# Kernel optimization log

Hardware: AMD Instinct MI355X
Metric: run time of the kernel (lower is better)

The kernel has to match this reference:

```python
import jax, jax.numpy as jnp
import numpy as np
import math

EMBED_DIM = 1024
NUM_HEADS = 16
HEAD_DIM = EMBED_DIM // NUM_HEADS


def setup_inputs() -> dict:
    key = jax.random.key(0)
    ks = jax.random.split(key, 5)
    x = jax.random.normal(ks[0], (4, 2048, EMBED_DIM), dtype=jnp.float32)
    # Linear params (torch nn.Linear: y = x @ W.T + b); init scale ~ 1/sqrt(fan_in)
    s = 1.0 / math.sqrt(EMBED_DIM)
    qkv_w = jax.random.uniform(ks[1], (3 * EMBED_DIM, EMBED_DIM), jnp.float32, -s, s)
    qkv_b = jax.random.uniform(ks[2], (3 * EMBED_DIM,), jnp.float32, -s, s)
    proj_w = jax.random.uniform(ks[3], (EMBED_DIM, EMBED_DIM), jnp.float32, -s, s)
    proj_b = jax.random.uniform(ks[4], (EMBED_DIM,), jnp.float32, -s, s)
    return {"x": x, "qkv_w": qkv_w, "qkv_b": qkv_b, "proj_w": proj_w, "proj_b": proj_b}


def reference(x, qkv_w, qkv_b, proj_w, proj_b):
    bsz, num_tokens, dim = x.shape
    qkv = x @ qkv_w.T + qkv_b  # [B, S, 3*D]
    qkv = qkv.reshape(bsz, num_tokens, 3, NUM_HEADS, HEAD_DIM)
    qkv = jnp.transpose(qkv, (2, 0, 3, 1, 4))  # [3, B, H, S, hd]
    q, k, v = qkv[0], qkv[1], qkv[2]
    scale = 1.0 / math.sqrt(HEAD_DIM)
    attn_scores = jnp.einsum('bhqd,bhkd->bhqk', q, k) * scale  # [B, H, S, S]
    attn = jax.nn.softmax(attn_scores, axis=-1)
    out = jnp.einsum('bhqk,bhkd->bhqd', attn, v)  # [B, H, S, hd]
    out = jnp.transpose(out, (0, 2, 1, 3)).reshape(bsz, num_tokens, dim)
    out = out @ proj_w.T + proj_b
    return out
```

## Files before the change

### kernel.cpp

```cpp
#include <hip/hip_runtime.h>
#include <stdint.h>

#define DEVICE static __device__ __forceinline__

typedef __bf16 bf16x8 __attribute__((ext_vector_type(8)));
typedef float f32x4 __attribute__((ext_vector_type(4)));

#define AS1 __attribute__((address_space(1)))
#define AS3 __attribute__((address_space(3)))

DEVICE void g2l16(const void* gptr, void* lptr) {
  __builtin_amdgcn_global_load_lds((AS1 uint32_t*)(uintptr_t)gptr,
                                   (AS3 uint32_t*)(uint32_t)(uintptr_t)lptr,
                                   16, 0, 0);
}

DEVICE float b2f(ushort h) {
  union { uint32_t u; float f; } v;
  v.u = ((uint32_t)h) << 16;
  return v.f;
}
DEVICE ushort f2b(float f) {
  union { float f; uint32_t u; } v;
  v.f = f;
  uint32_t u = v.u;
  return (ushort)((u + 0x7FFFu + ((u >> 16) & 1u)) >> 16);
}

#if defined(__has_builtin) && __has_builtin(__builtin_amdgcn_exp2f)
DEVICE float fast_exp2(float x) { return __builtin_amdgcn_exp2f(x); }
#else
extern "C" __device__ float __ocml_native_exp2_f32(float);
DEVICE float fast_exp2(float x) { return __ocml_native_exp2_f32(x); }
#endif

#define QSCALE 0.1803368801111244f

DEVICE int kperm(int x) {
  return (x & 0x23) | ((x & 0x18) >> 1) | ((x & 0x4) << 2);
}

__global__ void detect_dtype(const ushort* __restrict__ xu, int* __restrict__ flag) {
  __shared__ int bad;
  if (threadIdx.x == 0) bad = 0;
  __syncthreads();
  int mybad = 0;
#pragma unroll
  for (int j = 0; j < 8; ++j) {
    const int i = threadIdx.x * 8 + j;
    const ushort u = xu[2 * i];
    const int e = (u >> 7) & 0xFF;
    if (!(e == 0 || (e >= 96 && e <= 160))) mybad++;
  }
  atomicAdd(&bad, mybad);
  __syncthreads();
  if (threadIdx.x == 0) *flag = (bad > 512) ? 1 : 0;
}

__global__ void convert_bf16(const void* __restrict__ src, ushort* __restrict__ dst,
                             int n, const int* __restrict__ flag) {
  const bool isf32 = (*flag != 0);
  const int n8 = n >> 3;
  for (int i = blockIdx.x * blockDim.x + threadIdx.x; i < n8;
       i += gridDim.x * blockDim.x) {
    ushort pk[8];
    if (isf32) {
      const float4 a = ((const float4*)src)[2 * i];
      const float4 b = ((const float4*)src)[2 * i + 1];
      pk[0] = f2b(a.x); pk[1] = f2b(a.y); pk[2] = f2b(a.z); pk[3] = f2b(a.w);
      pk[4] = f2b(b.x); pk[5] = f2b(b.y); pk[6] = f2b(b.z); pk[7] = f2b(b.w);
      *(uint4*)&dst[8 * i] = *(const uint4*)pk;
    } else {
      *(uint4*)&dst[8 * i] = ((const uint4*)src)[i];
    }
  }
}

template <int MODE, int GN>
__global__ __launch_bounds__(256)
void gemm_bt(const ushort* __restrict__ A, const ushort* __restrict__ W,
             const ushort* __restrict__ bias, ushort* __restrict__ O0,
             ushort* __restrict__ O1, ushort* __restrict__ O2,
             int M, int N, int K, const int* __restrict__ flag)
{
  __shared__ union SM {
    struct { ushort As[128 * 64]; ushort Bs[128 * 64]; } s;
    ushort Ct[128 * 136];
  } sm;

  const int tid = threadIdx.x;
  const int lane = tid & 63;
  const int wave = tid >> 6;
  const int quad = lane >> 4;
  const int lo = lane & 15;

  const int lin = blockIdx.y * gridDim.x + blockIdx.x;
  const int per = GN * gridDim.y;
  const int grp = lin / per;
  const int w   = lin % per;
  const int bxn = grp * GN + (w % GN);
  const int bym = w / GN;
  const int m0 = bym * 128;
  const int n0 = bxn * 128;

  const int wm = (wave >> 1) * 64;
  const int wn = (wave & 1) * 64;

  f32x4 acc[4][4] = {};

  for (int k0 = 0; k0 < K; k0 += 64) {
    __syncthreads();
#pragma unroll
    for (int i = 0; i < 4; ++i) {
      const int c = tid + 256 * i;
      const int row = c >> 3;
      const int kc = (c & 7) << 3;
      g2l16(A + (size_t)(m0 + row) * K + k0 + kc,
            (char*)sm.s.As + ((wave << 6) + (i << 8)) * 16);
      g2l16(W + (size_t)(n0 + row) * K + k0 + kc,
            (char*)sm.s.Bs + ((wave << 6) + (i << 8)) * 16);
    }
    __syncthreads();

#pragma unroll
    for (int ks = 0; ks < 2; ++ks) {
      bf16x8 af[4], bfr[4];
#pragma unroll
      for (int t = 0; t < 4; ++t) {
        af[t]  = *(const bf16x8*)&sm.s.As[(wm + t * 16 + lo) * 64 + ks * 32 + quad * 8];
        bfr[t] = *(const bf16x8*)&sm.s.Bs[(wn + t * 16 + lo) * 64 + ks * 32 + quad * 8];
      }
#pragma unroll
      for (int mt = 0; mt < 4; ++mt)
#pragma unroll
        for (int nt = 0; nt < 4; ++nt)
          acc[mt][nt] = __builtin_amdgcn_mfma_f32_16x16x32_bf16(
              af[mt], bfr[nt], acc[mt][nt], 0, 0, 0);
    }
  }

  if (MODE == 0) {
    const int which = n0 >> 10;
    if (which == 2) {
#pragma unroll
      for (int nt = 0; nt < 4; ++nt) {
        const int n = n0 + wn + nt * 16 + lo;
        const float bv2 = b2f(bias[n]);
        const int h = (n >> 6) & 15;
        const int d = n & 63;
#pragma unroll
        for (int mt = 0; mt < 4; ++mt) {
          const int mb = m0 + wm + mt * 16 + quad * 4;
          const int b = mb >> 11, s0 = mb & 2047;
          ushort pk[4];
#pragma unroll
          for (int r = 0; r < 4; ++r) pk[r] = f2b(acc[mt][nt][r] + bv2);
          *(uint2*)&O2[((size_t)(b * 16 + h) * 64 + d) * 2048 + s0] =
              *(const uint2*)pk;
        }
      }
    } else {
      const float qs = (which == 0) ? QSCALE : 1.0f;
      ushort* __restrict__ dst = (which == 0) ? O0 : O1;
      __syncthreads();
#pragma unroll
      for (int nt = 0; nt < 4; ++nt) {
        const int n = n0 + wn + nt * 16 + lo;
        const float bv2 = b2f(bias[n]);
#pragma unroll
        for (int mt = 0; mt < 4; ++mt)
#pragma unroll
          for (int r = 0; r < 4; ++r)
            sm.Ct[(wm + mt * 16 + quad * 4 + r) * 136 + wn + nt * 16 + lo] =
                f2b((acc[mt][nt][r] + bv2) * qs);
      }
      __syncthreads();
#pragma unroll
      for (int i = 0; i < 8; ++i) {
        const int c = tid + 256 * i;
        const int nch = c & 15;
        const int ml = c >> 4;
        const int n = n0 + nch * 8;
        const int h = (n >> 6) & 15;
        const int d = n & 63;
        const int mg = m0 + ml;
        const int b = mg >> 11;
        int s = mg & 2047;
        if (which == 1) s = (s & ~63) | kperm(s & 63);
        const uint4 val = *(const uint4*)&sm.Ct[ml * 136 + nch * 8];
        *(uint4*)&dst[(((size_t)(b * 16 + h) * 2048 + s) << 6) + d] = val;
      }
    }
  } else {
    const bool f32out = (*flag != 0);
    float* Of = (float*)O0;
#pragma unroll
    for (int nt = 0; nt < 4; ++nt) {
      const int n = n0 + wn + nt * 16 + lo;
      const float bv2 = b2f(bias[n]);
#pragma unroll
      for (int mt = 0; mt < 4; ++mt)
#pragma unroll
        for (int r = 0; r < 4; ++r) {
          const int m = m0 + wm + mt * 16 + quad * 4 + r;
          const float val = acc[mt][nt][r] + bv2;
          if (f32out) Of[(size_t)m * N + n] = val;
          else        O0[(size_t)m * N + n] = f2b(val);
        }
    }
  }
}

__global__ __launch_bounds__(256, 4)
void attn_fwd(const ushort* __restrict__ qp, const ushort* __restrict__ kp,
              const ushort* __restrict__ vp, ushort* __restrict__ o)
{
  __shared__ ushort Qs[128 * 64];
  __shared__ ushort Ks[64 * 64];
  __shared__ ushort Vt[64 * 64];

  const int tid = threadIdx.x;
  const int lane = tid & 63;
  const int wave = tid >> 6;
  const int quad = lane >> 4;
  const int lo = lane & 15;
  const int bh = blockIdx.y;
  const int q0 = blockIdx.x * 128;

  const ushort* Qg = qp + (size_t)bh * 2048 * 64;
  const ushort* Kg = kp + (size_t)bh * 2048 * 64;
  const ushort* Vg = vp + (size_t)bh * 64 * 2048;

#pragma unroll
  for (int i = 0; i < 4; ++i) {
    const int c = tid + 256 * i;
    const int row = c >> 3;
    const int kc = (c & 7) << 3;
    g2l16(Qg + (size_t)(q0 + row) * 64 + kc,
          (char*)Qs + ((wave << 6) + (i << 8)) * 16);
  }
  __syncthreads();

  bf16x8 qf[2][2];
#pragma unroll
  for (int mt = 0; mt < 2; ++mt)
#pragma unroll
    for (int ks = 0; ks < 2; ++ks)
      qf[mt][ks] = *(const bf16x8*)&Qs[(wave * 32 + mt * 16 + lo) * 64 + ks * 32 + quad * 8];

  bf16x8 ones;
#pragma unroll
  for (int j = 0; j < 8; ++j) ones[j] = (__bf16)1.0f;

  f32x4 oacc[2][4] = {};
  f32x4 sumacc[2] = {};

  for (int j0 = 0; j0 < 2048; j0 += 64) {
    __syncthreads();
#pragma unroll
    for (int i = 0; i < 2; ++i) {
      const int c = tid + 256 * i;
      const int row = c >> 3;
      const int kc = (c & 7) << 3;
      g2l16(Kg + (size_t)(j0 + row) * 64 + kc,
            (char*)Ks + ((wave << 6) + (i << 8)) * 16);
      g2l16(Vg + (size_t)row * 2048 + j0 + kc,
            (char*)Vt + ((wave << 6) + (i << 8)) * 16);
    }
    __syncthreads();

    f32x4 sacc[2][4] = {};
#pragma unroll
    for (int ks = 0; ks < 2; ++ks) {
#pragma unroll
      for (int nt = 0; nt < 4; ++nt) {
        const bf16x8 kf = *(const bf16x8*)&Ks[(nt * 16 + lo) * 64 + ks * 32 + quad * 8];
#pragma unroll
        for (int mt = 0; mt < 2; ++mt)
          sacc[mt][nt] = __builtin_amdgcn_mfma_f32_16x16x32_bf16(
              kf, qf[mt][ks], sacc[mt][nt], 0, 0, 0);
      }
    }

    bf16x8 pfr[2][2];
#pragma unroll
    for (int mt = 0; mt < 2; ++mt) {
      float p[4][4];
#pragma unroll
      for (int nt = 0; nt < 4; ++nt)
#pragma unroll
        for (int r = 0; r < 4; ++r)
          p[nt][r] = fast_exp2(sacc[mt][nt][r]);
#pragma unroll
      for (int b = 0; b < 2; ++b)
#pragma unroll
        for (int h = 0; h < 2; ++h)
#pragma unroll
          for (int r = 0; r < 4; ++r)
            pfr[mt][b][4 * h + r] = (__bf16)p[2 * b + h][r];
    }

#pragma unroll
    for (int b = 0; b < 2; ++b) {
#pragma unroll
      for (int mt = 0; mt < 2; ++mt)
        sumacc[mt] = __builtin_amdgcn_mfma_f32_16x16x32_bf16(
            pfr[mt][b], ones, sumacc[mt], 0, 0, 0);
#pragma unroll
      for (int dt = 0; dt < 4; ++dt) {
        const bf16x8 vf = *(const bf16x8*)&Vt[(dt * 16 + lo) * 64 + b * 32 + quad * 8];
#pragma unroll
        for (int mt = 0; mt < 2; ++mt)
          oacc[mt][dt] = __builtin_amdgcn_mfma_f32_16x16x32_bf16(
              pfr[mt][b], vf, oacc[mt][dt], 0, 0, 0);
      }
    }
  }

  const int b_ = bh >> 4;
  const int h = bh & 15;
#pragma unroll
  for (int mt = 0; mt < 2; ++mt) {
#pragma unroll
    for (int r = 0; r < 4; ++r) {
      const float inv = 1.0f / sumacc[mt][r];
      const int srow = q0 + wave * 32 + mt * 16 + quad * 4 + r;
#pragma unroll
      for (int dt = 0; dt < 4; ++dt) {
        o[(((size_t)(b_ * 2048 + srow)) << 10) + h * 64 + dt * 16 + lo] =
            f2b(oacc[mt][dt][r] * inv);
      }
    }
  }
}

extern "C" void kernel_launch(void* const* d_in, const int* in_sizes, int n_in,
                              void* d_out, int out_size, void* d_ws, size_t ws_size,
                              hipStream_t stream) {
  const size_t N_X  = (size_t)4 * 2048 * 1024;
  const size_t N_WQ = (size_t)3072 * 1024;
  const size_t N_BQ = 3072;
  const size_t N_WP = (size_t)1024 * 1024;
  const size_t N_BP = 1024;
  const size_t HSD  = (size_t)64 * 2048 * 64;

  ushort* xb = (ushort*)d_ws;
  ushort* wq = xb + N_X;
  ushort* bq = wq + N_WQ;
  ushort* wp = bq + N_BQ;
  ushort* bp = wp + N_WP;
  ushort* qb = bp + N_BP;
  ushort* kb = qb + HSD;
  ushort* vb = kb + HSD;
  ushort* ab = vb + HSD;
  int* flag  = (int*)(ab + HSD);

  detect_dtype<<<1, 256, 0, stream>>>((const ushort*)d_in[0], flag);
  convert_bf16<<<1024, 256, 0, stream>>>(d_in[0], xb, (int)N_X, flag);
  convert_bf16<<<512, 256, 0, stream>>>(d_in[1], wq, (int)N_WQ, flag);
  convert_bf16<<<2, 256, 0, stream>>>(d_in[2], bq, (int)N_BQ, flag);
  convert_bf16<<<256, 256, 0, stream>>>(d_in[3], wp, (int)N_WP, flag);
  convert_bf16<<<1, 256, 0, stream>>>(d_in[4], bp, (int)N_BP, flag);

  gemm_bt<0, 6><<<dim3(24, 64), dim3(256), 0, stream>>>(
      xb, wq, bq, qb, kb, vb, 8192, 3072, 1024, flag);
  attn_fwd<<<dim3(16, 64), dim3(256), 0, stream>>>(qb, kb, vb, ab);
  gemm_bt<1, 4><<<dim3(8, 64), dim3(256), 0, stream>>>(
      ab, wp, bp, (ushort*)d_out, nullptr, nullptr, 8192, 1024, 1024, flag);
}
```

Measured before the change: 297.6 us.

## Rewrite GEMMs as 128x256 8-wave tiles with 4-stage LDS pipeline; fuse converts

The five conversion launches are merged into a single kernel that dispatches by global index range. Both GEMMs now use 512-thread blocks computing 128x256 tiles. The K loop uses BK=32 with a four-buffer LDS ring, prefetching two steps ahead and synchronising with explicit vmcnt waits and barriers, plus s_setprio around the MFMA blocks. The QKV epilogue now stages data per wave in LDS scratch instead of through a block-wide transpose buffer. The goal is to hide global-load latency and cut launch overhead, at the cost of fewer blocks in flight and a larger LDS footprint.

```diff
diff --git a/kernel.cpp b/kernel.cpp
--- a/kernel.cpp
+++ b/kernel.cpp
@@ -57,12 +57,22 @@
   if (threadIdx.x == 0) *flag = (bad > 512) ? 1 : 0;
 }
 
-__global__ void convert_bf16(const void* __restrict__ src, ushort* __restrict__ dst,
-                             int n, const int* __restrict__ flag) {
+__global__ void convert_all(const void* __restrict__ s0, const void* __restrict__ s1,
+                            const void* __restrict__ s2, const void* __restrict__ s3,
+                            const void* __restrict__ s4,
+                            ushort* __restrict__ d0, ushort* __restrict__ d1,
+                            ushort* __restrict__ d2, ushort* __restrict__ d3,
+                            ushort* __restrict__ d4,
+                            const int* __restrict__ flag) {
   const bool isf32 = (*flag != 0);
-  const int n8 = n >> 3;
-  for (int i = blockIdx.x * blockDim.x + threadIdx.x; i < n8;
-       i += gridDim.x * blockDim.x) {
+  for (int g = blockIdx.x * blockDim.x + threadIdx.x; g < 1573376;
+       g += gridDim.x * blockDim.x) {
+    const void* src; ushort* dst; int i;
+    if (g < 1048576)      { src = s0; dst = d0; i = g; }
+    else if (g < 1441792) { src = s1; dst = d1; i = g - 1048576; }
+    else if (g < 1442176) { src = s2; dst = d2; i = g - 1441792; }
+    else if (g < 1573248) { src = s3; dst = d3; i = g - 1442176; }
+    else                  { src = s4; dst = d4; i = g - 1573248; }
     ushort pk[8];
     if (isf32) {
       const float4 a = ((const float4*)src)[2 * i];
@@ -77,16 +87,13 @@
 }
 
 template <int MODE, int GN>
-__global__ __launch_bounds__(256)
-void gemm_bt(const ushort* __restrict__ A, const ushort* __restrict__ W,
+__global__ __launch_bounds__(512, 2)
+void gemm256(const ushort* __restrict__ A, const ushort* __restrict__ W,
              const ushort* __restrict__ bias, ushort* __restrict__ O0,
              ushort* __restrict__ O1, ushort* __restrict__ O2,
              int M, int N, int K, const int* __restrict__ flag)
 {
-  __shared__ union SM {
-    struct { ushort As[128 * 64]; ushort Bs[128 * 64]; } s;
-    ushort Ct[128 * 136];
-  } sm;
+  __shared__ __align__(16) char smem[98304];
 
   const int tid = threadIdx.x;
   const int lane = tid & 63;
@@ -101,41 +108,78 @@
   const int bxn = grp * GN + (w % GN);
   const int bym = w / GN;
   const int m0 = bym * 128;
-  const int n0 = bxn * 128;
-
-  const int wm = (wave >> 1) * 64;
-  const int wn = (wave & 1) * 64;
+  const int n0 = bxn * 256;
+
+  const int wm = (wave >> 2) * 64;
+  const int wn = (wave & 3) * 64;
+
+  const int rA = tid >> 2;
+  const int gA = (tid & 3) << 3;
+  const size_t offA  = (size_t)(m0 + rA) * K + gA;
+  const size_t offB0 = (size_t)(n0 + rA) * K + gA;
+  const size_t offB1 = (size_t)(n0 + 128 + rA) * K + gA;
+  const int dA = wave << 10;
+  const int NT = K >> 5;
 
   f32x4 acc[4][4] = {};
 
-  for (int k0 = 0; k0 < K; k0 += 64) {
-    __syncthreads();
-#pragma unroll
-    for (int i = 0; i < 4; ++i) {
-      const int c = tid + 256 * i;
-      const int row = c >> 3;
-      const int kc = (c & 7) << 3;
-      g2l16(A + (size_t)(m0 + row) * K + k0 + kc,
-            (char*)sm.s.As + ((wave << 6) + (i << 8)) * 16);
-      g2l16(W + (size_t)(n0 + row) * K + k0 + kc,
-            (char*)sm.s.Bs + ((wave << 6) + (i << 8)) * 16);
-    }
-    __syncthreads();
-
-#pragma unroll
-    for (int ks = 0; ks < 2; ++ks) {
-      bf16x8 af[4], bfr[4];
-#pragma unroll
-      for (int t = 0; t < 4; ++t) {
-        af[t]  = *(const bf16x8*)&sm.s.As[(wm + t * 16 + lo) * 64 + ks * 32 + quad * 8];
-        bfr[t] = *(const bf16x8*)&sm.s.Bs[(wn + t * 16 + lo) * 64 + ks * 32 + quad * 8];
-      }
-#pragma unroll
-      for (int mt = 0; mt < 4; ++mt)
-#pragma unroll
-        for (int nt = 0; nt < 4; ++nt)
-          acc[mt][nt] = __builtin_amdgcn_mfma_f32_16x16x32_bf16(
-              af[mt], bfr[nt], acc[mt][nt], 0, 0, 0);
+#pragma unroll
+  for (int t = 0; t < 2; ++t) {
+    char* buf = smem + t * 24576;
+    g2l16(A + offA  + t * 32, buf + dA);
+    g2l16(W + offB0 + t * 32, buf + 8192 + dA);
+    g2l16(W + offB1 + t * 32, buf + 16384 + dA);
+  }
+  asm volatile("s_waitcnt vmcnt(3)" ::: "memory");
+  __builtin_amdgcn_s_barrier();
+
+  for (int kt = 0; kt < NT; ++kt) {
+    const char* buf = smem + (kt & 3) * 24576;
+    const ushort* Al = (const ushort*)buf;
+    const ushort* Bl = (const ushort*)(buf + 8192);
+    const bool pf = (kt + 2 < NT);
+    char* nbuf = smem + ((kt + 2) & 3) * 24576;
+
+    if (pf) {
+      g2l16(A + offA  + (size_t)(kt + 2) * 32, nbuf + dA);
+      g2l16(W + offB0 + (size_t)(kt + 2) * 32, nbuf + 8192 + dA);
+    }
+    bf16x8 bfr[4], af[2];
+#pragma unroll
+    for (int nt = 0; nt < 4; ++nt)
+      bfr[nt] = *(const bf16x8*)&Bl[(wn + nt * 16 + lo) * 32 + quad * 8];
+#pragma unroll
+    for (int mt = 0; mt < 2; ++mt)
+      af[mt] = *(const bf16x8*)&Al[(wm + mt * 16 + lo) * 32 + quad * 8];
+    __builtin_amdgcn_s_setprio(1);
+#pragma unroll
+    for (int mt = 0; mt < 2; ++mt)
+#pragma unroll
+      for (int nt = 0; nt < 4; ++nt)
+        acc[mt][nt] = __builtin_amdgcn_mfma_f32_16x16x32_bf16(
+            af[mt], bfr[nt], acc[mt][nt], 0, 0, 0);
+    __builtin_amdgcn_s_setprio(0);
+    __builtin_amdgcn_s_barrier();
+
+    if (pf)
+      g2l16(W + offB1 + (size_t)(kt + 2) * 32, nbuf + 16384 + dA);
+    bf16x8 af2[2];
+#pragma unroll
+    for (int mt = 0; mt < 2; ++mt)
+      af2[mt] = *(const bf16x8*)&Al[(wm + (mt + 2) * 16 + lo) * 32 + quad * 8];
+    __builtin_amdgcn_s_setprio(1);
+#pragma unroll
+    for (int mt = 0; mt < 2; ++mt)
+#pragma unroll
+      for (int nt = 0; nt < 4; ++nt)
+        acc[mt + 2][nt] = __builtin_amdgcn_mfma_f32_16x16x32_bf16(
+            af2[mt], bfr[nt], acc[mt + 2][nt], 0, 0, 0);
+    __builtin_amdgcn_s_setprio(0);
+
+    if (kt < NT - 1) {
+      if (pf) asm volatile("s_waitcnt vmcnt(3)" ::: "memory");
+      else    asm volatile("s_waitcnt vmcnt(0)" ::: "memory");
+      __builtin_amdgcn_s_barrier();
     }
   }
 
@@ -145,16 +189,16 @@
 #pragma unroll
       for (int nt = 0; nt < 4; ++nt) {
         const int n = n0 + wn + nt * 16 + lo;
-        const float bv2 = b2f(bias[n]);
+        const float bv = b2f(bias[n]);
         const int h = (n >> 6) & 15;
         const int d = n & 63;
 #pragma unroll
         for (int mt = 0; mt < 4; ++mt) {
-          const int mb = m0 + wm + mt * 16 + quad * 4;
-          const int b = mb >> 11, s0 = mb & 2047;
+          const int m = m0 + wm + mt * 16 + quad * 4;
+          const int b = m >> 11, s0 = m & 2047;
           ushort pk[4];
 #pragma unroll
-          for (int r = 0; r < 4; ++r) pk[r] = f2b(acc[mt][nt][r] + bv2);
+          for (int r = 0; r < 4; ++r) pk[r] = f2b(acc[mt][nt][r] + bv);
           *(uint2*)&O2[((size_t)(b * 16 + h) * 64 + d) * 2048 + s0] =
               *(const uint2*)pk;
         }
@@ -162,33 +206,34 @@
     } else {
       const float qs = (which == 0) ? QSCALE : 1.0f;
       ushort* __restrict__ dst = (which == 0) ? O0 : O1;
+      const int h = ((n0 + wn) >> 6) & 15;
       __syncthreads();
-#pragma unroll
-      for (int nt = 0; nt < 4; ++nt) {
-        const int n = n0 + wn + nt * 16 + lo;
-        const float bv2 = b2f(bias[n]);
-#pragma unroll
-        for (int mt = 0; mt < 4; ++mt)
-#pragma unroll
-          for (int r = 0; r < 4; ++r)
-            sm.Ct[(wm + mt * 16 + quad * 4 + r) * 136 + wn + nt * 16 + lo] =
-                f2b((acc[mt][nt][r] + bv2) * qs);
-      }
-      __syncthreads();
-#pragma unroll
-      for (int i = 0; i < 8; ++i) {
-        const int c = tid + 256 * i;
-        const int nch = c & 15;
-        const int ml = c >> 4;
-        const int n = n0 + nch * 8;
-        const int h = (n >> 6) & 15;
-        const int d = n & 63;
-        const int mg = m0 + ml;
-        const int b = mg >> 11;
-        int s = mg & 2047;
-        if (which == 1) s = (s & ~63) | kperm(s & 63);
-        const uint4 val = *(const uint4*)&sm.Ct[ml * 136 + nch * 8];
-        *(uint4*)&dst[(((size_t)(b * 16 + h) * 2048 + s) << 6) + d] = val;
+      ushort* scr = (ushort*)(smem + wave * 12288);
+      float bv[4];
+#pragma unroll
+      for (int nt = 0; nt < 4; ++nt) bv[nt] = b2f(bias[n0 + wn + nt * 16 + lo]);
+#pragma unroll
+      for (int c2 = 0; c2 < 2; ++c2) {
+#pragma unroll
+        for (int mtl = 0; mtl < 2; ++mtl)
+#pragma unroll
+          for (int nt = 0; nt < 4; ++nt)
+#pragma unroll
+            for (int r = 0; r < 4; ++r)
+              scr[(mtl * 16 + quad * 4 + r) * 88 + nt * 16 + lo] =
+                  f2b((acc[c2 * 2 + mtl][nt][r] + bv[nt]) * qs);
+        asm volatile("s_waitcnt lgkmcnt(0)" ::: "memory");
+#pragma unroll
+        for (int i = 0; i < 4; ++i) {
+          const int id = lane + 64 * i;
+          const int rowl = id >> 3, nch = id & 7;
+          const uint4 val = *(const uint4*)&scr[rowl * 88 + nch * 8];
+          const int m = m0 + wm + c2 * 32 + rowl;
+          const int b = m >> 11;
+          int s = m & 2047;
+          if (which == 1) s = (s & ~63) | kperm(s & 63);
+          *(uint4*)&dst[((size_t)(b * 16 + h) * 2048 + s) * 64 + nch * 8] = val;
+        }
       }
     }
   } else {
@@ -197,13 +242,13 @@
 #pragma unroll
     for (int nt = 0; nt < 4; ++nt) {
       const int n = n0 + wn + nt * 16 + lo;
-      const float bv2 = b2f(bias[n]);
+      const float bv = b2f(bias[n]);
 #pragma unroll
       for (int mt = 0; mt < 4; ++mt)
 #pragma unroll
         for (int r = 0; r < 4; ++r) {
           const int m = m0 + wm + mt * 16 + quad * 4 + r;
-          const float val = acc[mt][nt][r] + bv2;
+          const float val = acc[mt][nt][r] + bv;
           if (f32out) Of[(size_t)m * N + n] = val;
           else        O0[(size_t)m * N + n] = f2b(val);
         }
@@ -356,15 +401,12 @@
   int* flag  = (int*)(ab + HSD);
 
   detect_dtype<<<1, 256, 0, stream>>>((const ushort*)d_in[0], flag);
-  convert_bf16<<<1024, 256, 0, stream>>>(d_in[0], xb, (int)N_X, flag);
-  convert_bf16<<<512, 256, 0, stream>>>(d_in[1], wq, (int)N_WQ, flag);
-  convert_bf16<<<2, 256, 0, stream>>>(d_in[2], bq, (int)N_BQ, flag);
-  convert_bf16<<<256, 256, 0, stream>>>(d_in[3], wp, (int)N_WP, flag);
-  convert_bf16<<<1, 256, 0, stream>>>(d_in[4], bp, (int)N_BP, flag);
-
-  gemm_bt<0, 6><<<dim3(24, 64), dim3(256), 0, stream>>>(
+  convert_all<<<2048, 256, 0, stream>>>(d_in[0], d_in[1], d_in[2], d_in[3], d_in[4],
+                                        xb, wq, bq, wp, bp, flag);
+
+  gemm256<0, 4><<<dim3(12, 64), dim3(512), 0, stream>>>(
       xb, wq, bq, qb, kb, vb, 8192, 3072, 1024, flag);
   attn_fwd<<<dim3(16, 64), dim3(256), 0, stream>>>(qb, kb, vb, ab);
-  gemm_bt<1, 4><<<dim3(8, 64), dim3(256), 0, stream>>>(
+  gemm256<1, 4><<<dim3(4, 64), dim3(512), 0, stream>>>(
       ab, wp, bp, (ushort*)d_out, nullptr, nullptr, 8192, 1024, 1024, flag);
 }
```

New measurement: 269.4 us. 9.5% less time.
